# Optimization experiments

Hardware: AMD Instinct MI355X
Metric: run time of the kernel (lower is better)

The kernel has to match this reference:

```python
import jax, jax.numpy as jnp
import numpy as np

B, N, K, D, H = 8, 128, 64, 256, 8  # batch, groups, keys-per-query, k_dim (=h_size), n_head


def setup_inputs() -> dict:
    key = jax.random.key(0)
    kq, kk, kv, kw, kb = jax.random.split(key, 5)
    bound = 1.0 / np.sqrt(D)  # torch nn.Bilinear default init bound
    return {
        "q": jax.random.normal(kq, (B, N, 1, D), jnp.float32),
        "k": jax.random.normal(kk, (B, N, K, D), jnp.float32),
        "v": jax.random.normal(kv, (B, N, K, D), jnp.float32),
        "W": jax.random.uniform(kw, (H, D, D), jnp.float32, -bound, bound),
        "b": jax.random.uniform(kb, (H,), jnp.float32, -bound, bound),
    }


def reference(q, k, v, W, b):
    Bs, Ns, Ks, Ds = k.shape
    Hh = W.shape[0]
    qe = q[:, :, 0, :]  # (B,N,D); torch expands q over K, einsum broadcasts instead
    # nn.Bilinear: scores[b,n,k,h] = q[b,n,:] @ W[h] @ k[b,n,k,:] + b[h]
    scores = jnp.einsum('bnd,hde,bnke->bnkh', qe, W, k) + b  # (B,N,K,H)
    # Faithful to torch's .view(B, N, -1, K): row-major reinterpretation of the
    # trailing (K, H) pair as (H, K) — a dim-mixing reshape, not a transpose.
    attn = scores.reshape(Bs, Ns, Hh, Ks)
    attn = jax.nn.softmax(attn, axis=-1)  # softmax over last dim (dropout p=0)
    # matmul(attn, v) -> (B,N,H,Dv); then sum over the head axis
    output = jnp.einsum('bnhk,bnkd->bnd', attn, v)
    return output, attn
```

## Files before the change

kernel.cpp:

```cpp
#include <hip/hip_runtime.h>
#include <math.h>

namespace {

constexpr int D = 256;
constexpr int H = 8;

typedef __attribute__((ext_vector_type(8))) short bf16x8;
typedef __attribute__((ext_vector_type(4))) float f32x4;

__device__ inline unsigned short bf16rn(float x) {
  unsigned u = __builtin_bit_cast(unsigned, x);
  u += 0x7fffu + ((u >> 16) & 1u);
  return (unsigned short)(u >> 16);
}
__device__ inline float bf16tof(unsigned short b) {
  return __builtin_bit_cast(float, (unsigned)b << 16);
}
__device__ inline void hilo8(const float* e, bf16x8& hv, bf16x8& lv) {
  #pragma unroll
  for (int p = 0; p < 8; ++p) {
    unsigned short h = bf16rn(e[p]);
    hv[p] = (short)h;
    lv[p] = (short)bf16rn(e[p] - bf16tof(h));
  }
}

__global__ __launch_bounds__(256) void qw_direct_kernel(
    const float* __restrict__ q, const float* __restrict__ W,
    unsigned short* __restrict__ qWb) {
  const int tid = threadIdx.x;
  const int w   = blockIdx.x * 4 + (tid >> 6);
  const int l   = tid & 63;
  const int bt  = w >> 6;
  const int hp  = w & 63;
  const int lrow  = l & 15;
  const int lcol8 = (l >> 4) << 3;

  f32x4 acc[2];
  acc[0] = f32x4{0.f, 0.f, 0.f, 0.f};
  acc[1] = f32x4{0.f, 0.f, 0.f, 0.f};

  const float* qbase = q + (size_t)(bt * 16 + lrow) * 256 + lcol8;

  #pragma unroll 2
  for (int ks = 0; ks < 8; ++ks) {
    float ea[8];
    {
      const float4 a0 = *reinterpret_cast<const float4*>(qbase + ks * 32);
      const float4 a1 = *reinterpret_cast<const float4*>(qbase + ks * 32 + 4);
      ea[0] = a0.x; ea[1] = a0.y; ea[2] = a0.z; ea[3] = a0.w;
      ea[4] = a1.x; ea[5] = a1.y; ea[6] = a1.z; ea[7] = a1.w;
    }
    bf16x8 aH, aL;
    hilo8(ea, aH, aL);

    #pragma unroll
    for (int j = 0; j < 2; ++j) {
      const int he = hp * 2 + j;
      const int h  = he >> 4, et = he & 15;
      const float* wp = W + (size_t)h * 65536 +
                        (size_t)(ks * 32 + lcol8) * 256 + et * 16 + lrow;
      float eb[8];
      #pragma unroll
      for (int jj = 0; jj < 8; ++jj) eb[jj] = wp[(size_t)jj * 256];
      bf16x8 bH, bL;
      hilo8(eb, bH, bL);
      acc[j] = __builtin_amdgcn_mfma_f32_16x16x32_bf16(aH, bH, acc[j], 0, 0, 0);
      acc[j] = __builtin_amdgcn_mfma_f32_16x16x32_bf16(aH, bL, acc[j], 0, 0, 0);
      acc[j] = __builtin_amdgcn_mfma_f32_16x16x32_bf16(aL, bH, acc[j], 0, 0, 0);
    }
  }

  const int rbase = (l >> 4) * 4;
  const int col   = l & 15;
  #pragma unroll
  for (int j = 0; j < 2; ++j) {
    const size_t cidx = (size_t)(hp * 2 + j) * 16 + col;
    #pragma unroll
    for (int r = 0; r < 4; ++r) {
      const int bn = bt * 16 + rbase + r;
      qWb[(size_t)bn * 2048 + cidx] = bf16rn(acc[j][r]);
    }
  }
}

constexpr int FB2   = 0;
constexpr int WSP2  = 8320;
constexpr int SMEM3 = 9344;

__global__ __launch_bounds__(256, 4) void attn_fused_kernel(
    const unsigned short* __restrict__ qWb, const float* __restrict__ kin,
    const float* __restrict__ vin, const float* __restrict__ bin,
    float* __restrict__ out, float* __restrict__ attn_out) {
  __shared__ alignas(16) long long smem_ll[SMEM3 / 8];
  char* sm = reinterpret_cast<char*>(smem_ll);
  float* wsp = reinterpret_cast<float*>(sm + WSP2);
  const int tid = threadIdx.x;
  const int bn  = blockIdx.x;
  const int wid = tid >> 6;
  const int ln  = tid & 63;

  const float* arow = kin + (size_t)bn * 16384 +
                      (size_t)(wid * 16 + (ln & 15)) * 256 + ((ln >> 4) << 3);
  float4 ka[16];
  #pragma unroll
  for (int ks = 0; ks < 8; ++ks) {
    ka[2 * ks]     = *reinterpret_cast<const float4*>(arow + ks * 32);
    ka[2 * ks + 1] = *reinterpret_cast<const float4*>(arow + ks * 32 + 4);
  }
  uint4 qh = *reinterpret_cast<const uint4*>(qWb + (size_t)bn * 2048 + tid * 8);

  {
    const int ks = tid >> 5, slot = 32 + (tid & 31);
    *reinterpret_cast<uint4*>(sm + FB2 + ks * 1040 + slot * 16) =
        make_uint4(0u, 0u, 0u, 0u);
  }
  #pragma unroll
  for (int i = 0; i < 2; ++i) {
    const int p = 2 * tid + i;
    const int hh = p >> 6, equad = p & 63;
    const int ks = equad >> 3, g = (equad >> 1) & 3, j0 = (equad & 1) * 4;
    const int base = FB2 + ks * 1040 + (hh * 4 + g) * 16 + j0 * 2;
    *reinterpret_cast<uint2*>(sm + base) =
        i == 0 ? make_uint2(qh.x, qh.y) : make_uint2(qh.z, qh.w);
  }
  __syncthreads();

  const int slot_r = (ln & 15) * 4 + (ln >> 4);
  const char* pbH = sm + FB2 + slot_r * 16;
  f32x4 acc = {0.f, 0.f, 0.f, 0.f};
  #pragma unroll
  for (int ks = 0; ks < 8; ++ks) {
    const float4 a0 = ka[2 * ks], a1 = ka[2 * ks + 1];
    bf16x8 aH;
    aH[0] = (short)bf16rn(a0.x); aH[1] = (short)bf16rn(a0.y);
    aH[2] = (short)bf16rn(a0.z); aH[3] = (short)bf16rn(a0.w);
    aH[4] = (short)bf16rn(a1.x); aH[5] = (short)bf16rn(a1.y);
    aH[6] = (short)bf16rn(a1.z); aH[7] = (short)bf16rn(a1.w);
    bf16x8 bH = *reinterpret_cast<const bf16x8*>(pbH + ks * 1040);
    acc = __builtin_amdgcn_mfma_f32_16x16x32_bf16(aH, bH, acc, 0, 0, 0);
  }

  const float bias = bin[ln & 7];
  const int col = ln & 15;
  const bool valid = col < 8;
  float x0 = acc[0] + bias, x1 = acc[1] + bias, x2 = acc[2] + bias, x3 = acc[3] + bias;
  float m = valid ? fmaxf(fmaxf(x0, x1), fmaxf(x2, x3)) : -1e30f;
  m = fmaxf(m, __shfl_xor(m, 1, 64));
  m = fmaxf(m, __shfl_xor(m, 2, 64));
  m = fmaxf(m, __shfl_xor(m, 4, 64));
  m = fmaxf(m, __shfl_xor(m, 16, 64));
  float e0 = valid ? expf(x0 - m) : 0.f;
  float e1 = valid ? expf(x1 - m) : 0.f;
  float e2 = valid ? expf(x2 - m) : 0.f;
  float e3 = valid ? expf(x3 - m) : 0.f;
  float s = e0 + e1 + e2 + e3;
  s += __shfl_xor(s, 1, 64);
  s += __shfl_xor(s, 2, 64);
  s += __shfl_xor(s, 4, 64);
  s += __shfl_xor(s, 16, 64);
  float inv = 1.f / s;
  float p0 = e0 * inv, p1 = e1 * inv, p2 = e2 * inv, p3 = e3 * inv;
  if (valid) {
    size_t base = (size_t)bn * 512 + (size_t)(wid * 16 + (ln >> 4) * 4) * 8 + col;
    attn_out[base]      = p0;
    attn_out[base + 8]  = p1;
    attn_out[base + 16] = p2;
    attn_out[base + 24] = p3;
  }
  p0 += __shfl_xor(p0, 32, 64);
  p1 += __shfl_xor(p1, 32, 64);
  p2 += __shfl_xor(p2, 32, 64);
  p3 += __shfl_xor(p3, 32, 64);
  if (ln < 32 && (ln & 15) < 8) {
    const int rb = (ln >> 4) * 4;
    const int c8 = ln & 7;
    float* w = wsp + wid * 64;
    w[(rb + 0) * 8 + c8] = p0;
    w[(rb + 1) * 8 + c8] = p1;
    w[(rb + 2) * 8 + c8] = p2;
    w[(rb + 3) * 8 + c8] = p3;
  }
  __syncthreads();

  const float4* v4 = reinterpret_cast<const float4*>(vin) + (size_t)bn * 4096;
  float4 av = make_float4(0.f, 0.f, 0.f, 0.f);
  #pragma unroll
  for (int i = 0; i < 16; ++i) {
    const int r = wid + 4 * i;
    float w = wsp[r] + wsp[64 + r] + wsp[128 + r] + wsp[192 + r];
    float4 vv = v4[r * 64 + ln];
    av.x += w * vv.x; av.y += w * vv.y; av.z += w * vv.z; av.w += w * vv.w;
  }
  float* s_red = reinterpret_cast<float*>(sm);
  *reinterpret_cast<float4*>(&s_red[wid * 260 + (ln << 2)]) = av;
  __syncthreads();

  out[(size_t)bn * D + tid] =
      s_red[tid] + s_red[260 + tid] + s_red[520 + tid] + s_red[780 + tid];
}

}

extern "C" void kernel_launch(void* const* d_in, const int* in_sizes, int n_in,
                              void* d_out, int out_size, void* d_ws, size_t ws_size,
                              hipStream_t stream) {
  const float* q = (const float*)d_in[0];
  const float* k = (const float*)d_in[1];
  const float* v = (const float*)d_in[2];
  const float* W = (const float*)d_in[3];
  const float* b = (const float*)d_in[4];

  float* out  = (float*)d_out;
  float* attn = out + 262144;
  unsigned short* qWb = (unsigned short*)d_ws;

  hipLaunchKernelGGL(qw_direct_kernel,  dim3(1024), dim3(256), 0, stream, q, W, qWb);
  hipLaunchKernelGGL(attn_fused_kernel, dim3(1024), dim3(256), 0, stream,
                     qWb, k, v, b, out, attn);
}
```

Measured before the change: 41.41 us.

## Stage K tiles into LDS via async global_load_lds and prefetch V early

The attention kernel now copies each block's 64 K rows straight into padded LDS rows using global_load_lds, rather than holding them in registers. It also issues all V loads into registers before the score MFMA and softmax, so K and V memory traffic overlap. The goal is to keep more bytes in flight in this bandwidth-bound kernel and hide V load latency behind the compute. In exchange, LDS use rises to about 75 KB per block and launch bounds drop from 4 to 2 blocks per CU, which lowers occupancy.

```diff
diff --git a/kernel.cpp b/kernel.cpp
--- a/kernel.cpp
+++ b/kernel.cpp
@@ -24,6 +24,11 @@
     hv[p] = (short)h;
     lv[p] = (short)bf16rn(e[p] - bf16tof(h));
   }
+}
+__device__ inline void async_copy16(float4* lds_dst, const float4* gsrc) {
+  __builtin_amdgcn_global_load_lds(
+      (const __attribute__((address_space(1))) unsigned int*)(gsrc),
+      (__attribute__((address_space(3))) unsigned int*)(lds_dst), 16, 0, 0);
 }
 
 __global__ __launch_bounds__(256) void qw_direct_kernel(
@@ -85,35 +90,40 @@
   }
 }
 
-constexpr int FB2   = 0;
-constexpr int WSP2  = 8320;
-constexpr int SMEM3 = 9344;
-
-__global__ __launch_bounds__(256, 4) void attn_fused_kernel(
+constexpr int KOFF   = 0;
+constexpr int BOFF   = 66560;
+constexpr int WSPOFF = 74880;
+constexpr int SMEM5  = 75904;
+
+__global__ __launch_bounds__(256, 2) void attn_fused_kernel(
     const unsigned short* __restrict__ qWb, const float* __restrict__ kin,
     const float* __restrict__ vin, const float* __restrict__ bin,
     float* __restrict__ out, float* __restrict__ attn_out) {
-  __shared__ alignas(16) long long smem_ll[SMEM3 / 8];
+  __shared__ alignas(16) long long smem_ll[SMEM5 / 8];
   char* sm = reinterpret_cast<char*>(smem_ll);
-  float* wsp = reinterpret_cast<float*>(sm + WSP2);
+  float* wsp = reinterpret_cast<float*>(sm + WSPOFF);
   const int tid = threadIdx.x;
   const int bn  = blockIdx.x;
   const int wid = tid >> 6;
   const int ln  = tid & 63;
 
-  const float* arow = kin + (size_t)bn * 16384 +
-                      (size_t)(wid * 16 + (ln & 15)) * 256 + ((ln >> 4) << 3);
-  float4 ka[16];
-  #pragma unroll
-  for (int ks = 0; ks < 8; ++ks) {
-    ka[2 * ks]     = *reinterpret_cast<const float4*>(arow + ks * 32);
-    ka[2 * ks + 1] = *reinterpret_cast<const float4*>(arow + ks * 32 + 4);
+  {
+    const float4* kb4 = reinterpret_cast<const float4*>(
+        kin + (size_t)bn * 16384 + (size_t)(wid * 16) * 256);
+    char* kdst = sm + KOFF + (size_t)(wid * 16) * 1040;
+    #pragma unroll
+    for (int i = 0; i < 16; ++i)
+      async_copy16(reinterpret_cast<float4*>(kdst + i * 1040), kb4 + i * 64 + ln);
   }
   uint4 qh = *reinterpret_cast<const uint4*>(qWb + (size_t)bn * 2048 + tid * 8);
+  const float4* v4 = reinterpret_cast<const float4*>(vin) + (size_t)bn * 4096;
+  float4 vv[16];
+  #pragma unroll
+  for (int i = 0; i < 16; ++i) vv[i] = v4[(size_t)(wid + 4 * i) * 64 + ln];
 
   {
     const int ks = tid >> 5, slot = 32 + (tid & 31);
-    *reinterpret_cast<uint4*>(sm + FB2 + ks * 1040 + slot * 16) =
+    *reinterpret_cast<uint4*>(sm + BOFF + ks * 1040 + slot * 16) =
         make_uint4(0u, 0u, 0u, 0u);
   }
   #pragma unroll
@@ -121,23 +131,25 @@
     const int p = 2 * tid + i;
     const int hh = p >> 6, equad = p & 63;
     const int ks = equad >> 3, g = (equad >> 1) & 3, j0 = (equad & 1) * 4;
-    const int base = FB2 + ks * 1040 + (hh * 4 + g) * 16 + j0 * 2;
+    const int base = BOFF + ks * 1040 + (hh * 4 + g) * 16 + j0 * 2;
     *reinterpret_cast<uint2*>(sm + base) =
         i == 0 ? make_uint2(qh.x, qh.y) : make_uint2(qh.z, qh.w);
   }
   __syncthreads();
 
   const int slot_r = (ln & 15) * 4 + (ln >> 4);
-  const char* pbH = sm + FB2 + slot_r * 16;
+  const char* pbH = sm + BOFF + slot_r * 16;
+  const char* ar  = sm + KOFF + (size_t)(wid * 16 + (ln & 15)) * 1040 + ((ln >> 4) << 5);
   f32x4 acc = {0.f, 0.f, 0.f, 0.f};
   #pragma unroll
   for (int ks = 0; ks < 8; ++ks) {
-    const float4 a0 = ka[2 * ks], a1 = ka[2 * ks + 1];
+    f32x4 a0 = *reinterpret_cast<const f32x4*>(ar + ks * 128);
+    f32x4 a1 = *reinterpret_cast<const f32x4*>(ar + ks * 128 + 16);
     bf16x8 aH;
-    aH[0] = (short)bf16rn(a0.x); aH[1] = (short)bf16rn(a0.y);
-    aH[2] = (short)bf16rn(a0.z); aH[3] = (short)bf16rn(a0.w);
-    aH[4] = (short)bf16rn(a1.x); aH[5] = (short)bf16rn(a1.y);
-    aH[6] = (short)bf16rn(a1.z); aH[7] = (short)bf16rn(a1.w);
+    aH[0] = (short)bf16rn(a0[0]); aH[1] = (short)bf16rn(a0[1]);
+    aH[2] = (short)bf16rn(a0[2]); aH[3] = (short)bf16rn(a0[3]);
+    aH[4] = (short)bf16rn(a1[0]); aH[5] = (short)bf16rn(a1[1]);
+    aH[6] = (short)bf16rn(a1[2]); aH[7] = (short)bf16rn(a1[3]);
     bf16x8 bH = *reinterpret_cast<const bf16x8*>(pbH + ks * 1040);
     acc = __builtin_amdgcn_mfma_f32_16x16x32_bf16(aH, bH, acc, 0, 0, 0);
   }
@@ -184,14 +196,13 @@
   }
   __syncthreads();
 
-  const float4* v4 = reinterpret_cast<const float4*>(vin) + (size_t)bn * 4096;
   float4 av = make_float4(0.f, 0.f, 0.f, 0.f);
   #pragma unroll
   for (int i = 0; i < 16; ++i) {
     const int r = wid + 4 * i;
     float w = wsp[r] + wsp[64 + r] + wsp[128 + r] + wsp[192 + r];
-    float4 vv = v4[r * 64 + ln];
-    av.x += w * vv.x; av.y += w * vv.y; av.z += w * vv.z; av.w += w * vv.w;
+    av.x += w * vv[i].x; av.y += w * vv[i].y;
+    av.z += w * vv[i].z; av.w += w * vv[i].w;
   }
   float* s_red = reinterpret_cast<float*>(sm);
   *reinterpret_cast<float4*>(&s_red[wid * 260 + (ln << 2)]) = av;
```

Measured after the change: 44.63 us. +7.8%, slower.
